# Kernel tuning notes

Hardware: AMD Instinct MI355X
Metric: run time of the kernel (lower is better)

The kernel has to match this reference:

```python
import jax, jax.numpy as jnp
import numpy as np

B, X, Y, Z, CIN = 4, 64, 64, 64, 32
COUT = 32
MX, MY, MZ = 16, 16, 16


def setup_inputs() -> dict:
    key = jax.random.key(0)
    k1, k2, k3 = jax.random.split(key, 3)
    x = jax.random.normal(k1, (B, X, Y, Z, CIN), dtype=jnp.float32)
    # Glorot-uniform-like scale for (in, out, mx, my, mz) weights
    fan = CIN + COUT
    lim = np.sqrt(6.0 / fan).astype(np.float32)
    w_real = jax.random.uniform(k2, (CIN, COUT, MX, MY, MZ), minval=-lim, maxval=lim, dtype=jnp.float32)
    w_imag = jax.random.uniform(k3, (CIN, COUT, MX, MY, MZ), minval=-lim, maxval=lim, dtype=jnp.float32)
    return {"x": x, "w_real": w_real, "w_imag": w_imag}


def reference(x, w_real, w_imag):
    # tf.signal.fft3d transforms the innermost 3 axes of the 5D input:
    # x is [B, X, Y, Z, C] so the FFT runs over (Y, Z, C) -- faithful to source.
    x_ft = jnp.fft.fftn(x.astype(jnp.complex64), axes=(-3, -2, -1))
    x_ft = jnp.transpose(x_ft, (0, 4, 1, 2, 3))            # [B, C, X, Y, Z]
    mx, my, mz = w_real.shape[2], w_real.shape[3], w_real.shape[4]
    x_crop = x_ft[:, :, :mx, :my, :mz]                     # [B, Cin, mx, my, mz]
    w = jax.lax.complex(w_real, w_imag)                    # [Cin, Cout, mx, my, mz]
    out_ft = jnp.einsum('bixyz,ioxyz->boxyz', x_crop, w)   # [B, Cout, mx, my, mz]
    sx, sy, sz = x.shape[1], x.shape[2], x.shape[3]
    out_ft = jnp.pad(out_ft, ((0, 0), (0, 0), (0, sx - mx), (0, sy - my), (0, sz - mz)))
    out_ft = jnp.transpose(out_ft, (0, 2, 3, 4, 1))        # [B, X, Y, Z, Cout]
    x_out = jnp.fft.ifftn(out_ft, axes=(-3, -2, -1))
    return jnp.real(x_out)
```

## Files before the change

kernel.cpp:

```cpp
#include <hip/hip_runtime.h>
#include <math.h>

#define PI_F 3.14159265358979323846f


__global__ __launch_bounds__(256) void k_dft_z(const float* __restrict__ x,
                                               float2* __restrict__ T1) {
    int bid = blockIdx.x;
    int ih = bid & 1, yg = (bid >> 1) & 7, xx = (bid >> 4) & 15, b = bid >> 8;
    __shared__ float  sx[8192];
    __shared__ float2 twt[1024];
    float4* sx4 = (float4*)sx;
    const float4* src4 = (const float4*)(x + (size_t)((b * 64 + xx) * 64 + yg * 8) * 2048) + ih * 4;
    #pragma unroll
    for (int t = threadIdx.x; t < 2048; t += 256) {
        int i4 = t & 3, z = (t >> 2) & 63, y = t >> 8;
        sx4[(y * 64 + z) * 4 + i4] = src4[(size_t)y * 512 + z * 8 + i4];
    }
    const float cn = -2.0f * PI_F / 64.0f;
    for (int t = threadIdx.x; t < 1024; t += 256) {
        int z = t >> 4, kz = t & 15;
        float s, c; sincosf(cn * (float)((z * kz) & 63), &s, &c);
        twt[t] = make_float2(c, s);
    }
    __syncthreads();
    int ig = threadIdx.x & 3, kz2 = (threadIdx.x >> 2) & 7, y8 = threadIdx.x >> 5;
    float ar0[4], ai0[4], ar1[4], ai1[4];
    #pragma unroll
    for (int j = 0; j < 4; j++) { ar0[j] = ai0[j] = ar1[j] = ai1[j] = 0.f; }
    const float4* twv = (const float4*)twt;
    #pragma unroll 8
    for (int z = 0; z < 64; z++) {
        float4 va = sx4[(y8 * 64 + z) * 4 + ig];
        float4 tp = twv[z * 8 + kz2];
        float v[4] = {va.x, va.y, va.z, va.w};
        #pragma unroll
        for (int j = 0; j < 4; j++) {
            ar0[j] = fmaf(v[j], tp.x, ar0[j]);
            ai0[j] = fmaf(v[j], tp.y, ai0[j]);
            ar1[j] = fmaf(v[j], tp.z, ar1[j]);
            ai1[j] = fmaf(v[j], tp.w, ai1[j]);
        }
    }
    int y = yg * 8 + y8, kz0 = kz2 * 2, i0 = ih * 16 + ig * 4;
    float2* dst = T1 + (size_t)((b * 16 + xx) * 64 + y) * 512;
    float4* d0 = (float4*)(dst + kz0 * 32 + i0);
    d0[0] = make_float4(ar0[0], ai0[0], ar0[1], ai0[1]);
    d0[1] = make_float4(ar0[2], ai0[2], ar0[3], ai0[3]);
    float4* d1 = (float4*)(dst + (kz0 + 1) * 32 + i0);
    d1[0] = make_float4(ar1[0], ai1[0], ar1[1], ai1[1]);
    d1[1] = make_float4(ar1[2], ai1[2], ar1[3], ai1[3]);
}

__global__ __launch_bounds__(256) void k_dft_y(const float2* __restrict__ T1,
                                               float2* __restrict__ XH) {
    int bid = blockIdx.x;
    int ih = bid & 1, kzg = (bid >> 1) & 7, xx = (bid >> 4) & 15, b = bid >> 8;
    __shared__ float4 sT4[2 * 576];
    __shared__ float2 twt[1024];
    const float4* Tg4 = (const float4*)T1;
    size_t gbase = (size_t)(b * 16 + xx) * 64 * 256;
    #pragma unroll
    for (int t = threadIdx.x; t < 1024; t += 256) {
        int i4 = t & 7, kzl = (t >> 3) & 1, y = t >> 4;
        sT4[kzl * 576 + y * 9 + i4] =
            Tg4[gbase + (size_t)y * 256 + (kzg * 2 + kzl) * 16 + ih * 8 + i4];
    }
    const float cn = -2.0f * PI_F / 64.0f;
    for (int t = threadIdx.x; t < 1024; t += 256) {
        int y = t >> 4, ky = t & 15;
        float s, c; sincosf(cn * (float)((y * ky) & 63), &s, &c);
        twt[t] = make_float2(c, s);
    }
    __syncthreads();
    int ig = threadIdx.x & 7, kzl = (threadIdx.x >> 3) & 1, ky = threadIdx.x >> 4;
    float ar0 = 0.f, ai0 = 0.f, ar1 = 0.f, ai1 = 0.f;
    #pragma unroll 8
    for (int y = 0; y < 64; y++) {
        float4 a  = sT4[kzl * 576 + y * 9 + ig];
        float2 tp = twt[y * 16 + ky];
        ar0 += a.x * tp.x - a.y * tp.y;
        ai0 += a.x * tp.y + a.y * tp.x;
        ar1 += a.z * tp.x - a.w * tp.y;
        ai1 += a.z * tp.y + a.w * tp.x;
    }
    int kz = kzg * 2 + kzl;
    float2* dp = XH + (((size_t)(b * 16 + xx) * 16 + ky) * 16 + kz) * 32 + ih * 16 + ig * 2;
    *(float4*)dp = make_float4(ar0, ai0, ar1, ai1);
}

__global__ __launch_bounds__(512) void k_mid(const float2* __restrict__ XH,
                                             const float* __restrict__ wr,
                                             const float* __restrict__ wi,
                                             float2* __restrict__ G) {
    int bid = blockIdx.x;
    int ky = bid & 15, xx = bid >> 4;
    __shared__ float2 sA[4 * 528];
    __shared__ float2 sB[4 * 576];
    __shared__ float2 twt[1024];
    for (int t = threadIdx.x; t < 2048; t += 512) {
        int b = t >> 9, kz = (t >> 5) & 15, i = t & 31;
        sA[b * 528 + kz * 33 + i] =
            XH[(((size_t)(b * 16 + xx) * 16 + ky) * 16 + kz) * 32 + i];
    }
    const float cn32 = -2.0f * PI_F / 32.0f;
    for (int t = threadIdx.x; t < 1024; t += 512) {
        int m = t >> 5, k = t & 31;
        float s, c; sincosf(cn32 * (float)((m * k) & 31), &s, &c);
        twt[t] = make_float2(c, s);
    }
    __syncthreads();
    const float4* twv = (const float4*)twt;
    {
        int kz = threadIdx.x & 15, kig = (threadIdx.x >> 4) & 7, b = threadIdx.x >> 7;
        float xr[4], xi[4];
        #pragma unroll
        for (int j = 0; j < 4; j++) { xr[j] = xi[j] = 0.f; }
        #pragma unroll 8
        for (int i = 0; i < 32; i++) {
            float2 a   = sA[b * 528 + kz * 33 + i];
            float4 tp0 = twv[i * 16 + kig * 2];
            float4 tp1 = twv[i * 16 + kig * 2 + 1];
            xr[0] += a.x * tp0.x - a.y * tp0.y;  xi[0] += a.x * tp0.y + a.y * tp0.x;
            xr[1] += a.x * tp0.z - a.y * tp0.w;  xi[1] += a.x * tp0.w + a.y * tp0.z;
            xr[2] += a.x * tp1.x - a.y * tp1.y;  xi[2] += a.x * tp1.y + a.y * tp1.x;
            xr[3] += a.x * tp1.z - a.y * tp1.w;  xi[3] += a.x * tp1.w + a.y * tp1.z;
        }
        #pragma unroll
        for (int j = 0; j < 4; j++)
            sB[b * 576 + (kig * 4 + j) * 18 + kz] = make_float2(xr[j], xi[j]);
    }
    __syncthreads();
    {
        int kzg = threadIdx.x & 3, o = (threadIdx.x >> 2) & 31, b = threadIdx.x >> 7;
        int wbase = xx * 256 + ky * 16 + kzg * 4;
        float Fr[4], Fi[4];
        #pragma unroll
        for (int q = 0; q < 4; q++) { Fr[q] = Fi[q] = 0.f; }
        const float4* sB4 = (const float4*)sB;
        #pragma unroll 4
        for (int ki = 0; ki < 32; ki++) {
            float4 a01 = sB4[b * 288 + ki * 9 + kzg * 2];
            float4 a23 = sB4[b * 288 + ki * 9 + kzg * 2 + 1];
            float4 w4r = *(const float4*)(wr + (size_t)(ki * 32 + o) * 4096 + wbase);
            float4 w4i = *(const float4*)(wi + (size_t)(ki * 32 + o) * 4096 + wbase);
            float xr[4]  = {a01.x, a01.z, a23.x, a23.z};
            float xi[4]  = {a01.y, a01.w, a23.y, a23.w};
            float wrv[4] = {w4r.x, w4r.y, w4r.z, w4r.w};
            float wiv[4] = {w4i.x, w4i.y, w4i.z, w4i.w};
            #pragma unroll
            for (int q = 0; q < 4; q++) {
                Fr[q] += xr[q] * wrv[q] - xi[q] * wiv[q];
                Fi[q] += xr[q] * wiv[q] + xi[q] * wrv[q];
            }
        }
        #pragma unroll
        for (int q = 0; q < 4; q++) {
            int kz = kzg * 4 + q;
            sA[b * 528 + kz * 33 + o] = make_float2(Fr[q], Fi[q]);
        }
    }
    __syncthreads();
    {
        int kz = threadIdx.x & 15, cog = (threadIdx.x >> 4) & 7, b = threadIdx.x >> 7;
        float gr[4], gi[4];
        #pragma unroll
        for (int j = 0; j < 4; j++) { gr[j] = gi[j] = 0.f; }
        #pragma unroll 8
        for (int o = 0; o < 32; o++) {
            float2 f   = sA[b * 528 + kz * 33 + o];
            float4 tp0 = twv[o * 16 + cog * 2];
            float4 tp1 = twv[o * 16 + cog * 2 + 1];
            gr[0] += f.x * tp0.x + f.y * tp0.y;  gi[0] += f.y * tp0.x - f.x * tp0.y;
            gr[1] += f.x * tp0.z + f.y * tp0.w;  gi[1] += f.y * tp0.z - f.x * tp0.w;
            gr[2] += f.x * tp1.x + f.y * tp1.y;  gi[2] += f.y * tp1.x - f.x * tp1.y;
            gr[3] += f.x * tp1.z + f.y * tp1.w;  gi[3] += f.y * tp1.z - f.x * tp1.w;
        }
        float2* dp = G + (((size_t)(b * 16 + xx) * 16 + ky) * 16 + kz) * 32 + cog * 4;
        ((float4*)dp)[0] = make_float4(gr[0], gi[0], gr[1], gi[1]);
        ((float4*)dp)[1] = make_float4(gr[2], gi[2], gr[3], gi[3]);
    }
}

__global__ __launch_bounds__(256) void k_idft_zy(const float2* __restrict__ G,
                                                 float* __restrict__ out) {
    int bid = blockIdx.x;
    int ch = bid & 1, zc = (bid >> 1) & 7, xx = (bid >> 4) & 15, b = bid >> 8;
    float* dstb = out + (size_t)(b * 64 + xx) * 131072;
    __shared__ float2 sH[128 * 18];
    __shared__ float2 twy[1024];
    __shared__ float2 twz[8 * 17];
    const float cp = 2.0f * PI_F / 64.0f;
    for (int t = threadIdx.x; t < 1024; t += 256) {
        int ky = t >> 6, y = t & 63;
        float s, c; sincosf(cp * (float)((ky * y) & 63), &s, &c);
        twy[t] = make_float2(c, s);
    }
    if (threadIdx.x < 128) {
        int dz = threadIdx.x >> 4, kz = threadIdx.x & 15;
        int z = zc * 8 + dz;
        float s, c; sincosf(cp * (float)((kz * z) & 63), &s, &c);
        twz[dz * 17 + kz] = make_float2(c, s);
    }
    __syncthreads();
    {
        int coq = threadIdx.x & 1, dz = (threadIdx.x >> 1) & 7, ky = threadIdx.x >> 4;
        const float2* Gb = G + ((size_t)(b * 16 + xx) * 16 + ky) * 512 + ch * 16 + coq * 8;
        float Hr[8], Hi[8];
        #pragma unroll
        for (int j = 0; j < 8; j++) { Hr[j] = Hi[j] = 0.f; }
        #pragma unroll 4
        for (int kz = 0; kz < 16; kz++) {
            float2 tz = twz[dz * 17 + kz];
            #pragma unroll
            for (int k = 0; k < 4; k++) {
                float4 g = *(const float4*)(Gb + kz * 32 + k * 2);
                Hr[2 * k]     += g.x * tz.x - g.y * tz.y;
                Hi[2 * k]     += g.x * tz.y + g.y * tz.x;
                Hr[2 * k + 1] += g.z * tz.x - g.w * tz.y;
                Hi[2 * k + 1] += g.z * tz.y + g.w * tz.x;
            }
        }
        float2* hp = sH + (ky * 8 + dz) * 18 + coq * 8;
        #pragma unroll
        for (int k = 0; k < 4; k++)
            *(float4*)(hp + k * 2) = make_float4(Hr[2 * k], Hi[2 * k], Hr[2 * k + 1], Hi[2 * k + 1]);
    }
    __syncthreads();
    {
        int cog = threadIdx.x & 1, dz = (threadIdx.x >> 1) & 7, yg = threadIdx.x >> 4;
        float acc[4][8];
        #pragma unroll
        for (int yl = 0; yl < 4; yl++)
            #pragma unroll
            for (int cl = 0; cl < 8; cl++) acc[yl][cl] = 0.f;
        const float4* twy4 = (const float4*)twy;
        const float4* sH4 = (const float4*)sH;
        for (int ky = 0; ky < 16; ky++) {
            float4 t0 = twy4[ky * 32 + yg * 2 + 0];
            float4 t1 = twy4[ky * 32 + yg * 2 + 1];
            float4 h0 = sH4[(ky * 8 + dz) * 9 + cog * 4 + 0];
            float4 h1 = sH4[(ky * 8 + dz) * 9 + cog * 4 + 1];
            float4 h2 = sH4[(ky * 8 + dz) * 9 + cog * 4 + 2];
            float4 h3 = sH4[(ky * 8 + dz) * 9 + cog * 4 + 3];
            float tc[4] = {t0.x, t0.z, t1.x, t1.z};
            float ts[4] = {t0.y, t0.w, t1.y, t1.w};
            float hr[8] = {h0.x, h0.z, h1.x, h1.z, h2.x, h2.z, h3.x, h3.z};
            float hi[8] = {h0.y, h0.w, h1.y, h1.w, h2.y, h2.w, h3.y, h3.w};
            #pragma unroll
            for (int yl = 0; yl < 4; yl++)
                #pragma unroll
                for (int cl = 0; cl < 8; cl++)
                    acc[yl][cl] += tc[yl] * hr[cl] - ts[yl] * hi[cl];
        }
        const float sc = 1.0f / 131072.0f;
        #pragma unroll
        for (int yl = 0; yl < 4; yl++) {
            int y = yg * 4 + yl;
            float4* d4 = (float4*)(dstb + ((size_t)y * 64 + zc * 8 + dz) * 32 + ch * 16 + cog * 8);
            d4[0] = make_float4(acc[yl][0] * sc, acc[yl][1] * sc, acc[yl][2] * sc, acc[yl][3] * sc);
            d4[1] = make_float4(acc[yl][4] * sc, acc[yl][5] * sc, acc[yl][6] * sc, acc[yl][7] * sc);
        }
    }
}

extern "C" void kernel_launch(void* const* d_in, const int* in_sizes, int n_in,
                              void* d_out, int out_size, void* d_ws, size_t ws_size,
                              hipStream_t stream) {
    const float* x  = (const float*)d_in[0];
    const float* wr = (const float*)d_in[1];
    const float* wi = (const float*)d_in[2];
    float* out = (float*)d_out;
    char*  ws  = (char*)d_ws;
    float2* T1 = (float2*)ws;
    float2* XH = (float2*)(ws + (size_t)16777216);
    float2* Gb = (float2*)(ws + (size_t)16777216 + 4194304);

    for (int b = 0; b < 4; ++b)
        hipMemsetAsync(out + ((size_t)b * 64 + 16) * 131072, 0,
                       (size_t)48 * 131072 * sizeof(float), stream);

    k_dft_z  <<<1024, 256, 0, stream>>>(x, T1);
    k_dft_y  <<<1024, 256, 0, stream>>>(T1, XH);
    k_mid    <<< 256, 512, 0, stream>>>(XH, wr, wi, Gb);
    k_idft_zy<<<1024, 256, 0, stream>>>(Gb, out);
}
```

Baseline: 308.7 us.

## Fuse output zero-fill into mid kernel and register-block DFT-y over two ky

Replaces the four hipMemsetAsync calls with extra blocks appended to the k_mid launch that zero the untouched output region, cutting separate launch overhead and letting the fill overlap the mid stage. k_dft_y now has each thread compute two ky outputs for four kz per block, halving the grid and reusing each loaded input element across two twiddles. The change costs more registers and shared memory per block, and the zero-fill blocks run in the same launch as the compute blocks.

After: 288.8 us. -6.5%, faster.

```diff
diff --git a/kernel.cpp b/kernel.cpp
--- a/kernel.cpp
+++ b/kernel.cpp
@@ -55,16 +55,16 @@
 __global__ __launch_bounds__(256) void k_dft_y(const float2* __restrict__ T1,
                                                float2* __restrict__ XH) {
     int bid = blockIdx.x;
-    int ih = bid & 1, kzg = (bid >> 1) & 7, xx = (bid >> 4) & 15, b = bid >> 8;
-    __shared__ float4 sT4[2 * 576];
+    int ih = bid & 1, kzg = (bid >> 1) & 3, xx = (bid >> 3) & 15, b = bid >> 7;
+    __shared__ float4 sT4[2304];
     __shared__ float2 twt[1024];
     const float4* Tg4 = (const float4*)T1;
     size_t gbase = (size_t)(b * 16 + xx) * 64 * 256;
     #pragma unroll
-    for (int t = threadIdx.x; t < 1024; t += 256) {
-        int i4 = t & 7, kzl = (t >> 3) & 1, y = t >> 4;
-        sT4[kzl * 576 + y * 9 + i4] =
-            Tg4[gbase + (size_t)y * 256 + (kzg * 2 + kzl) * 16 + ih * 8 + i4];
+    for (int t = threadIdx.x; t < 2048; t += 256) {
+        int i4 = t & 7, kz4 = (t >> 3) & 3, y = t >> 5;
+        sT4[kz4 * 576 + y * 9 + i4] =
+            Tg4[gbase + (size_t)y * 256 + (kzg * 4 + kz4) * 16 + ih * 8 + i4];
     }
     const float cn = -2.0f * PI_F / 64.0f;
     for (int t = threadIdx.x; t < 1024; t += 256) {
@@ -73,27 +73,48 @@
         twt[t] = make_float2(c, s);
     }
     __syncthreads();
-    int ig = threadIdx.x & 7, kzl = (threadIdx.x >> 3) & 1, ky = threadIdx.x >> 4;
-    float ar0 = 0.f, ai0 = 0.f, ar1 = 0.f, ai1 = 0.f;
+    int ig = threadIdx.x & 7, ky2 = (threadIdx.x >> 3) & 7, kz4 = threadIdx.x >> 6;
+    float ar[2][2], ai[2][2];
+    #pragma unroll
+    for (int h = 0; h < 2; h++) { ar[h][0] = ar[h][1] = ai[h][0] = ai[h][1] = 0.f; }
+    const float4* twv = (const float4*)twt;
     #pragma unroll 8
     for (int y = 0; y < 64; y++) {
-        float4 a  = sT4[kzl * 576 + y * 9 + ig];
-        float2 tp = twt[y * 16 + ky];
-        ar0 += a.x * tp.x - a.y * tp.y;
-        ai0 += a.x * tp.y + a.y * tp.x;
-        ar1 += a.z * tp.x - a.w * tp.y;
-        ai1 += a.z * tp.y + a.w * tp.x;
-    }
-    int kz = kzg * 2 + kzl;
-    float2* dp = XH + (((size_t)(b * 16 + xx) * 16 + ky) * 16 + kz) * 32 + ih * 16 + ig * 2;
-    *(float4*)dp = make_float4(ar0, ai0, ar1, ai1);
+        float4 a  = sT4[kz4 * 576 + y * 9 + ig];
+        float4 tp = twv[y * 8 + ky2];
+        float xr[2] = {a.x, a.z}, xi[2] = {a.y, a.w};
+        #pragma unroll
+        for (int j = 0; j < 2; j++) {
+            ar[0][j] += xr[j] * tp.x - xi[j] * tp.y;
+            ai[0][j] += xr[j] * tp.y + xi[j] * tp.x;
+            ar[1][j] += xr[j] * tp.z - xi[j] * tp.w;
+            ai[1][j] += xr[j] * tp.w + xi[j] * tp.z;
+        }
+    }
+    int kz = kzg * 4 + kz4;
+    #pragma unroll
+    for (int h = 0; h < 2; h++) {
+        int ky = ky2 * 2 + h;
+        float2* dp = XH + (((size_t)(b * 16 + xx) * 16 + ky) * 16 + kz) * 32 + ih * 16 + ig * 2;
+        *(float4*)dp = make_float4(ar[h][0], ai[h][0], ar[h][1], ai[h][1]);
+    }
 }
 
 __global__ __launch_bounds__(512) void k_mid(const float2* __restrict__ XH,
                                              const float* __restrict__ wr,
                                              const float* __restrict__ wi,
-                                             float2* __restrict__ G) {
+                                             float2* __restrict__ G,
+                                             float* __restrict__ out) {
     int bid = blockIdx.x;
+    if (bid >= 256) {
+        int f = bid - 256;
+        int b = f / 384, rem = f - b * 384;
+        float4* d4 = (float4*)(out + (size_t)(b * 64 + 16) * 131072) + (size_t)rem * 4096;
+        #pragma unroll
+        for (int r = 0; r < 8; ++r)
+            d4[r * 512 + threadIdx.x] = make_float4(0.f, 0.f, 0.f, 0.f);
+        return;
+    }
     int ky = bid & 15, xx = bid >> 4;
     __shared__ float2 sA[4 * 528];
     __shared__ float2 sB[4 * 576];
@@ -276,12 +297,8 @@
     float2* XH = (float2*)(ws + (size_t)16777216);
     float2* Gb = (float2*)(ws + (size_t)16777216 + 4194304);
 
-    for (int b = 0; b < 4; ++b)
-        hipMemsetAsync(out + ((size_t)b * 64 + 16) * 131072, 0,
-                       (size_t)48 * 131072 * sizeof(float), stream);
-
     k_dft_z  <<<1024, 256, 0, stream>>>(x, T1);
-    k_dft_y  <<<1024, 256, 0, stream>>>(T1, XH);
-    k_mid    <<< 256, 512, 0, stream>>>(XH, wr, wi, Gb);
+    k_dft_y  <<< 512, 256, 0, stream>>>(T1, XH);
+    k_mid    <<<1792, 512, 0, stream>>>(XH, wr, wi, Gb, out);
     k_idft_zy<<<1024, 256, 0, stream>>>(Gb, out);
 }
```
